# Optimization experiments

Hardware: AMD Instinct MI355X
Metric: run time of the kernel (lower is better)

## Reference

```python
import jax, jax.numpy as jnp
import numpy as np

N = 100000      # nodes
E = 1600000     # edges (avg degree 16)
N_IN, N_HID, N_OUT = 512, 256, 64
HOP = 10


def setup_inputs() -> dict:
    key = jax.random.key(0)
    k = jax.random.split(key, 8)
    x = jax.random.normal(k[0], (N, N_IN), dtype=jnp.float32)
    edge_row = jax.random.randint(k[1], (E,), 0, N, dtype=jnp.int64)
    edge_col = jax.random.randint(k[2], (E,), 0, N, dtype=jnp.int64)
    # values ~ 1/avg_degree, mimicking normalized adjacency
    edge_vals = jax.random.uniform(k[3], (E,), dtype=jnp.float32) * 0.0625
    W1 = jax.random.normal(k[4], (N_HID, N_IN), dtype=jnp.float32) * (1.0 / np.sqrt(N_IN))
    b1 = jnp.zeros((N_HID,), dtype=jnp.float32)
    W2 = jax.random.normal(k[5], (N_OUT, N_HID), dtype=jnp.float32) * (1.0 / np.sqrt(N_HID))
    b2 = jnp.zeros((N_OUT,), dtype=jnp.float32)
    s = jax.random.normal(k[6], (N_OUT, 1), dtype=jnp.float32) * 0.1
    return {"x": x, "edge_row": edge_row, "edge_col": edge_col,
            "edge_vals": edge_vals, "W1": W1, "b1": b1, "W2": W2,
            "b2": b2, "s": s}


def reference(x, edge_row, edge_col, edge_vals, W1, b1, W2, b2, s):
    # MLP transform (dropout=0 / eval mode)
    h = jax.nn.relu(x @ W1.T + b1)          # [N, N_HID]
    h = h @ W2.T + b2                        # [N, N_OUT]
    # multi-hop sparse propagation: h_{k+1} = A @ h_k  (COO SpMM)
    outs = [h]
    for _ in range(HOP):
        msg = edge_vals[:, None] * h[edge_col]                       # [E, N_OUT]
        h = jax.ops.segment_sum(msg, edge_row, num_segments=N)       # [N, N_OUT]
        outs.append(h)
    H = jnp.stack(outs, axis=1)              # [N, HOP+1, N_OUT]
    # sigmoid hop-attention: S = sigmoid(H @ s), out = S^T H
    S = jax.nn.sigmoid(jnp.einsum('nkf,fo->nk', H, s))  # [N, HOP+1]
    out = jnp.einsum('nk,nkf->nf', S, H)     # [N, N_OUT]
    return out
```

## Files before the change

kernel.cpp:

```cpp
#include <hip/hip_runtime.h>
#include <hip/hip_bf16.h>

#define NIN  512
#define NHID 256
#define NOUT 64
#define HOPS 10

typedef __attribute__((ext_vector_type(8))) short bf16x8;
typedef __attribute__((ext_vector_type(4))) float f32x4;

__device__ __forceinline__ unsigned short f2bf(float f) {
    unsigned u = __float_as_uint(f);
    u += 0x7FFFu + ((u >> 16) & 1u);
    return (unsigned short)(u >> 16);
}
__device__ __forceinline__ unsigned pk2(float a, float b) {
    return (unsigned)f2bf(a) | ((unsigned)f2bf(b) << 16);
}
__device__ __forceinline__ float bflo(unsigned g) { return __uint_as_float(g << 16); }
__device__ __forceinline__ float bfhi(unsigned g) { return __uint_as_float(g & 0xFFFF0000u); }

__global__ void k_preconv(const float* __restrict__ W1, const float* __restrict__ W2,
                          unsigned short* __restrict__ W1f, unsigned short* __restrict__ W2f)
{
    const int i = blockIdx.x * 256 + threadIdx.x;
    if (i < NHID * NIN) {
        const int j = i & 7, l = (i >> 3) & 63, fi = i >> 9;
        const int ks = fi >> 4, w = (fi >> 2) & 3, nf = fi & 3;
        const int col = w * 64 + nf * 16 + (l & 15);
        const int k   = ks * 32 + ((l >> 4) << 3) + j;
        W1f[i] = f2bf(W1[col * NIN + k]);
    }
    if (i < NOUT * NHID) {
        const int j = i & 7, l = (i >> 3) & 63, fi = i >> 9;
        const int ks = fi >> 2, nf = fi & 3;
        const int col = nf * 16 + (l & 15);
        const int k   = ks * 32 + ((j >> 2) << 4) + ((l >> 4) << 2) + (j & 3);
        W2f[i] = f2bf(W2[col * NHID + k]);
    }
}

__global__ __launch_bounds__(256, 2) void mlp_kernel(
    const float* __restrict__ x, const unsigned short* __restrict__ W1f,
    const float* __restrict__ b1, const unsigned short* __restrict__ W2f,
    const float* __restrict__ b2, const float* __restrict__ s,
    unsigned* __restrict__ hpack, float* __restrict__ sigbuf, int n)
{
    __shared__ __align__(16) char smem[50432];
    short* B2L  = (short*)smem;
    short* BX   = (short*)(smem + 32768);
    float* H0L  = (float*)(smem + 32768);
    float* SIGL = (float*)(smem + 50176);

    const int t  = threadIdx.x;
    const int w  = t >> 6, lz = t & 63;
    const int row0 = blockIdx.x * 64;

    const int srow = t >> 2;
    int xrow = row0 + srow; if (xrow >= n) xrow = n - 1;
    const float4* xp = (const float4*)(x + (size_t)xrow * NIN);
    const int q4a = t & 3, q4b = (t & 3) + 4;

    f32x4 acc[4][4];
    #pragma unroll
    for (int a = 0; a < 4; ++a)
        #pragma unroll
        for (int b = 0; b < 4; ++b) acc[a][b] = (f32x4)(0.f);

    auto xwrite = [&](int b, float4 va, float4 vb) {
        unsigned long long pa = (unsigned long long)pk2(va.x, va.y)
                              | ((unsigned long long)pk2(va.z, va.w) << 32);
        unsigned long long pb = (unsigned long long)pk2(vb.x, vb.y)
                              | ((unsigned long long)pk2(vb.z, vb.w) << 32);
        *(unsigned long long*)&BX[(((((b << 2) + (srow >> 4)) << 6)
            + ((srow & 15) | ((q4a >> 1) << 4))) << 3) + ((q4a & 1) << 2)] = pa;
        *(unsigned long long*)&BX[(((((b << 2) + (srow >> 4)) << 6)
            + ((srow & 15) | ((q4b >> 1) << 4))) << 3) + ((q4b & 1) << 2)] = pb;
    };
    auto compute = [&](int b, int kt) {
        bf16x8 xf[4], wf[4];
        #pragma unroll
        for (int nfn = 0; nfn < 4; ++nfn)
            xf[nfn] = *(const bf16x8*)&BX[((((b << 2) + nfn) << 6) + lz) << 3];
        const unsigned short* wp = W1f + ((size_t)kt << 13) + (w << 11) + (lz << 3);
        #pragma unroll
        for (int hf = 0; hf < 4; ++hf)
            wf[hf] = *(const bf16x8*)(wp + (hf << 9));
        #pragma unroll
        for (int nfn = 0; nfn < 4; ++nfn)
            #pragma unroll
            for (int hf = 0; hf < 4; ++hf)
                acc[nfn][hf] = __builtin_amdgcn_mfma_f32_16x16x32_bf16(
                    wf[hf], xf[nfn], acc[nfn][hf], 0, 0, 0);
    };

    {
        float4 xa = xp[q4a], xb = xp[q4b];
        xwrite(0, xa, xb);
    }
    __syncthreads();

    #pragma unroll 1
    for (int kt = 0; kt < 16; ++kt) {
        const int b = kt & 1;
        float4 nxa, nxb;
        if (kt < 15) {
            nxa = xp[((kt + 1) << 3) + q4a];
            nxb = xp[((kt + 1) << 3) + q4b];
        }
        compute(b, kt);
        if (kt < 15) xwrite(b ^ 1, nxa, nxb);
        __syncthreads();
    }

    {
        float4 b1q[4];
        #pragma unroll
        for (int hf = 0; hf < 4; ++hf)
            b1q[hf] = *(const float4*)(b1 + (w << 6) + (hf << 4) + ((lz >> 4) << 2));
        #pragma unroll
        for (int nfn = 0; nfn < 4; ++nfn) {
            #pragma unroll
            for (int cl = 0; cl < 2; ++cl) {
                f32x4 a0 = acc[nfn][2 * cl], a1 = acc[nfn][2 * cl + 1];
                float4 c0 = b1q[2 * cl], c1 = b1q[2 * cl + 1];
                uint4 pv;
                pv.x = pk2(fmaxf(a0.x + c0.x, 0.f), fmaxf(a0.y + c0.y, 0.f));
                pv.y = pk2(fmaxf(a0.z + c0.z, 0.f), fmaxf(a0.w + c0.w, 0.f));
                pv.z = pk2(fmaxf(a1.x + c1.x, 0.f), fmaxf(a1.y + c1.y, 0.f));
                pv.w = pk2(fmaxf(a1.z + c1.z, 0.f), fmaxf(a1.w + c1.w, 0.f));
                *(uint4*)&B2L[((((nfn << 3) + (w << 1) + cl) << 6) + lz) << 3] = pv;
            }
        }
    }
    __syncthreads();

    f32x4 acc2[4];
    #pragma unroll
    for (int nf2 = 0; nf2 < 4; ++nf2) acc2[nf2] = (f32x4)(0.f);

    #pragma unroll
    for (int c = 0; c < 8; ++c) {
        bf16x8 hfrag = *(const bf16x8*)&B2L[((((w << 3) + c) << 6) + lz) << 3];
        #pragma unroll
        for (int nf2 = 0; nf2 < 4; ++nf2) {
            bf16x8 wfrag = *(const bf16x8*)(W2f + (((c << 2) + nf2) << 9) + (lz << 3));
            acc2[nf2] = __builtin_amdgcn_mfma_f32_16x16x32_bf16(
                wfrag, hfrag, acc2[nf2], 0, 0, 0);
        }
    }

    {
        float dot = 0.f;
        #pragma unroll
        for (int nf2 = 0; nf2 < 4; ++nf2) {
            float4 bq = *(const float4*)(b2 + (nf2 << 4) + ((lz >> 4) << 2));
            float4 qv = *(const float4*)(s  + (nf2 << 4) + ((lz >> 4) << 2));
            acc2[nf2].x += bq.x; acc2[nf2].y += bq.y;
            acc2[nf2].z += bq.z; acc2[nf2].w += bq.w;
            dot += acc2[nf2].x * qv.x + acc2[nf2].y * qv.y
                 + acc2[nf2].z * qv.z + acc2[nf2].w * qv.w;
        }
        dot += __shfl_xor(dot, 16);
        dot += __shfl_xor(dot, 32);
        const float sig = 1.f / (1.f + expf(-dot));
        if (lz < 16) SIGL[(w << 4) + lz] = sig;
        const int mloc = (w << 4) + (lz & 15);
        #pragma unroll
        for (int nf2 = 0; nf2 < 4; ++nf2) {
            float4 hv; hv.x = acc2[nf2].x; hv.y = acc2[nf2].y;
            hv.z = acc2[nf2].z; hv.w = acc2[nf2].w;
            *(float4*)&H0L[mloc * 68 + (nf2 << 4) + ((lz >> 4) << 2)] = hv;
        }
    }
    __syncthreads();

    {
        const int m = t >> 2, q = t & 3;
        const int g = row0 + m;
        if (g < n) {
            unsigned* hp = hpack + (size_t)g * 32 + (q << 3);
            #pragma unroll
            for (int i = 0; i < 16; i += 4) {
                float4 hv = *(const float4*)&H0L[m * 68 + (q << 4) + i];
                uint2 pv;
                pv.x = pk2(hv.x, hv.y);
                pv.y = pk2(hv.z, hv.w);
                *(uint2*)(hp + (i >> 1)) = pv;
            }
        }
        if (t < 64 && row0 + t < n) sigbuf[row0 + t] = SIGL[t];
    }
}

__global__ void k_count(const int* __restrict__ erow, int* __restrict__ deg, int e) {
    int i = blockIdx.x * 256 + threadIdx.x;
    if (i < e) atomicAdd(&deg[erow[i]], 1);
}

__global__ void k_scan1(const int* __restrict__ deg, int* __restrict__ rp,
                        int* __restrict__ bsum, int nv) {
    __shared__ int sm[256];
    const int i = blockIdx.x * 256 + threadIdx.x;
    const int v = (i < nv) ? deg[i] : 0;
    sm[threadIdx.x] = v;
    __syncthreads();
    for (int off = 1; off < 256; off <<= 1) {
        int tv = (threadIdx.x >= off) ? sm[threadIdx.x - off] : 0;
        __syncthreads();
        sm[threadIdx.x] += tv;
        __syncthreads();
    }
    if (i < nv) rp[i] = sm[threadIdx.x] - v;
    if (threadIdx.x == 255) bsum[blockIdx.x] = sm[255];
}

__global__ void k_scan2(int* __restrict__ bsum, int nb) {
    __shared__ int sm[512];
    const int tid = threadIdx.x;
    const int v = (tid < nb) ? bsum[tid] : 0;
    sm[tid] = v;
    __syncthreads();
    for (int off = 1; off < 512; off <<= 1) {
        int tv = (tid >= off) ? sm[tid - off] : 0;
        __syncthreads();
        sm[tid] += tv;
        __syncthreads();
    }
    if (tid < nb) bsum[tid] = sm[tid] - v;
}

__global__ void k_scan3(int* __restrict__ rp, int* __restrict__ cur,
                        const int* __restrict__ bsum, int nv, int e) {
    const int i = blockIdx.x * 256 + threadIdx.x;
    if (i < nv) {
        const int vv = rp[i] + bsum[blockIdx.x];
        rp[i]  = vv;
        cur[i] = vv;
    }
    if (i == 0) rp[nv] = e;
}

__global__ void k_scatter(const int* __restrict__ erow, const int* __restrict__ ecol,
                          const float* __restrict__ ev, int* __restrict__ cur,
                          unsigned long long* __restrict__ cpack, int e) {
    const int i = blockIdx.x * 256 + threadIdx.x;
    if (i < e) {
        const int r = erow[i];
        const int p = atomicAdd(&cur[r], 1);
        cpack[p] = ((unsigned long long)__float_as_uint(ev[i]) << 32)
                 | (unsigned)ecol[i];
    }
}

__global__ __launch_bounds__(256) void hop_kernel(
    const unsigned* __restrict__ h_in, unsigned* __restrict__ h_out,
    const int* __restrict__ row_ptr, const unsigned long long* __restrict__ cpack,
    const float* __restrict__ s, float* __restrict__ sig_out, int n)
{
    const int t  = threadIdx.x;
    const int sl = t & 31;
    const int node = (blockIdx.x * 256 + t) >> 5;
    if (node >= n) return;
    const int start = row_ptr[node];
    const int end   = row_ptr[node + 1];
    float a0 = 0.f, a1 = 0.f;
    for (int base = start; base < end; base += 32) {
        const int idx = base + sl;
        unsigned long long pc = (idx < end) ? cpack[idx] : 0ULL;
        int   c = (int)(unsigned)pc;
        float v = __uint_as_float((unsigned)(pc >> 32));
        const int cnt = min(32, end - base);
        int e = 0;
        for (; e + 4 <= cnt; e += 4) {
            int   c0 = __shfl(c, e, 32),     c1 = __shfl(c, e + 1, 32);
            int   c2 = __shfl(c, e + 2, 32), c3 = __shfl(c, e + 3, 32);
            float v0 = __shfl(v, e, 32),     v1 = __shfl(v, e + 1, 32);
            float v2 = __shfl(v, e + 2, 32), v3 = __shfl(v, e + 3, 32);
            unsigned g0 = h_in[(size_t)c0 * 32 + sl];
            unsigned g1 = h_in[(size_t)c1 * 32 + sl];
            unsigned g2 = h_in[(size_t)c2 * 32 + sl];
            unsigned g3 = h_in[(size_t)c3 * 32 + sl];
            a0 = fmaf(v0, bflo(g0), a0); a1 = fmaf(v0, bfhi(g0), a1);
            a0 = fmaf(v1, bflo(g1), a0); a1 = fmaf(v1, bfhi(g1), a1);
            a0 = fmaf(v2, bflo(g2), a0); a1 = fmaf(v2, bfhi(g2), a1);
            a0 = fmaf(v3, bflo(g3), a0); a1 = fmaf(v3, bfhi(g3), a1);
        }
        for (; e < cnt; ++e) {
            int   cc = __shfl(c, e, 32);
            float vv = __shfl(v, e, 32);
            unsigned g = h_in[(size_t)cc * 32 + sl];
            a0 = fmaf(vv, bflo(g), a0); a1 = fmaf(vv, bfhi(g), a1);
        }
    }
    const float2 sv = ((const float2*)s)[sl];
    float tv = a0 * sv.x + a1 * sv.y;
    #pragma unroll
    for (int off = 16; off > 0; off >>= 1) tv += __shfl_xor(tv, off, 32);
    h_out[(size_t)node * 32 + sl] = pk2(a0, a1);
    if (sl == 0) sig_out[node] = 1.f / (1.f + expf(-tv));
}

__global__ __launch_bounds__(256) void k_combine(
    const unsigned* __restrict__ hbuf, const float* __restrict__ sigbuf,
    float* __restrict__ out, int n)
{
    const int gid  = blockIdx.x * 256 + threadIdx.x;
    const int node = gid >> 5, sl = gid & 31;
    if (node >= n) return;
    float o0 = 0.f, o1 = 0.f;
    #pragma unroll
    for (int k = 0; k <= HOPS; ++k) {
        const unsigned g = hbuf[(size_t)k * n * 32 + (size_t)node * 32 + sl];
        const float sg = sigbuf[(size_t)k * n + node];
        o0 = fmaf(sg, bflo(g), o0);
        o1 = fmaf(sg, bfhi(g), o1);
    }
    float2 ov; ov.x = o0; ov.y = o1;
    ((float2*)out)[(size_t)node * 32 + sl] = ov;
}

extern "C" void kernel_launch(void* const* d_in, const int* in_sizes, int n_in,
                              void* d_out, int out_size, void* d_ws, size_t ws_size,
                              hipStream_t stream)
{
    const float* x  = (const float*)d_in[0];
    const int*   er = (const int*)  d_in[1];
    const int*   ec = (const int*)  d_in[2];
    const float* ev = (const float*)d_in[3];
    const float* W1 = (const float*)d_in[4];
    const float* b1 = (const float*)d_in[5];
    const float* W2 = (const float*)d_in[6];
    const float* b2 = (const float*)d_in[7];
    const float* s  = (const float*)d_in[8];
    float* out = (float*)d_out;

    const int n = in_sizes[0] / NIN;
    const int e = in_sizes[1];

    char* w = (char*)d_ws;
    auto carve = [&](size_t bytes) { char* p = w; w += (bytes + 255) & ~(size_t)255; return p; };
    unsigned* hbuf   = (unsigned*)carve((size_t)(HOPS + 1) * n * 32 * 4);
    float*    sigbuf = (float*)   carve((size_t)(HOPS + 1) * n * 4);
    int*      deg    = (int*)     carve((size_t)n * 4);
    int*      rp     = (int*)     carve(((size_t)n + 1) * 4);
    int*      cur    = (int*)     carve((size_t)n * 4);
    unsigned long long* cpack = (unsigned long long*)carve((size_t)e * 8);
    int*      bsum   = (int*)     carve(1024 * 4);
    unsigned short* W1f = (unsigned short*)carve((size_t)NHID * NIN * 2);
    unsigned short* W2f = (unsigned short*)carve((size_t)NOUT * NHID * 2);

    hipMemsetAsync(deg, 0, (size_t)n * 4, stream);

    k_preconv<<<(NHID * NIN + 255) / 256, 256, 0, stream>>>(W1, W2, W1f, W2f);

    const int mgrid = (n + 63) / 64;
    mlp_kernel<<<mgrid, 256, 0, stream>>>(x, W1f, b1, W2f, b2, s,
                                          hbuf, sigbuf, n);

    const int eg = (e + 255) / 256;
    const int nb = (n + 255) / 256;
    k_count  <<<eg, 256, 0, stream>>>(er, deg, e);
    k_scan1  <<<nb, 256, 0, stream>>>(deg, rp, bsum, n);
    k_scan2  <<<1, 512, 0, stream>>>(bsum, nb);
    k_scan3  <<<nb, 256, 0, stream>>>(rp, cur, bsum, n, e);
    k_scatter<<<eg, 256, 0, stream>>>(er, ec, ev, cur, cpack, e);

    const int hgrid = ((size_t)n * 32 + 255) / 256;
    for (int hop = 0; hop < HOPS; ++hop) {
        hop_kernel<<<hgrid, 256, 0, stream>>>(
            hbuf + (size_t)hop * n * 32, hbuf + (size_t)(hop + 1) * n * 32,
            rp, cpack, s, sigbuf + (size_t)(hop + 1) * n, n);
    }

    k_combine<<<hgrid, 256, 0, stream>>>(hbuf, sigbuf, out, n);
}
```

Before: 626.0 us.

## Bucket edges by row range before CSR scatter to localize atomics and writes

Builds the CSR with a two-pass scatter. Edges are first appended into 64 coarse row buckets (2048 rows each) using block-local histograms and per-bucket global cursors. The fine atomic scatter into cpack then walks this bucketed stream, so its atomics and writes touch a small row window at a time instead of random addresses. The cost is an extra 16-byte-per-edge intermediate buffer and one more pass over the edges. The change also raises the MLP kernel's launch-bounds occupancy hint from 2 to 3, which may increase register pressure.

```diff
diff --git a/kernel.cpp b/kernel.cpp
--- a/kernel.cpp
+++ b/kernel.cpp
@@ -5,6 +5,7 @@
 #define NHID 256
 #define NOUT 64
 #define HOPS 10
+#define NB   64
 
 typedef __attribute__((ext_vector_type(8))) short bf16x8;
 typedef __attribute__((ext_vector_type(4))) float f32x4;
@@ -40,7 +41,7 @@
     }
 }
 
-__global__ __launch_bounds__(256, 2) void mlp_kernel(
+__global__ __launch_bounds__(256, 3) void mlp_kernel(
     const float* __restrict__ x, const unsigned short* __restrict__ W1f,
     const float* __restrict__ b1, const unsigned short* __restrict__ W2f,
     const float* __restrict__ b2, const float* __restrict__ s,
@@ -193,9 +194,20 @@
     }
 }
 
-__global__ void k_count(const int* __restrict__ erow, int* __restrict__ deg, int e) {
-    int i = blockIdx.x * 256 + threadIdx.x;
-    if (i < e) atomicAdd(&deg[erow[i]], 1);
+__global__ void k_count_hist(const int* __restrict__ erow, int* __restrict__ deg,
+                             int* __restrict__ bcnt, int e) {
+    __shared__ int lh[NB];
+    const int t = threadIdx.x;
+    if (t < NB) lh[t] = 0;
+    __syncthreads();
+    const int i = blockIdx.x * 256 + t;
+    if (i < e) {
+        const int r = erow[i];
+        atomicAdd(&deg[r], 1);
+        atomicAdd(&lh[r >> 11], 1);
+    }
+    __syncthreads();
+    if (t < NB && lh[t]) atomicAdd(&bcnt[t], lh[t]);
 }
 
 __global__ void k_scan1(const int* __restrict__ deg, int* __restrict__ rp,
@@ -215,7 +227,8 @@
     if (threadIdx.x == 255) bsum[blockIdx.x] = sm[255];
 }
 
-__global__ void k_scan2(int* __restrict__ bsum, int nb) {
+__global__ void k_scan2(int* __restrict__ bsum, int nb,
+                        const int* __restrict__ bcnt, int* __restrict__ bcur) {
     __shared__ int sm[512];
     const int tid = threadIdx.x;
     const int v = (tid < nb) ? bsum[tid] : 0;
@@ -228,6 +241,16 @@
         __syncthreads();
     }
     if (tid < nb) bsum[tid] = sm[tid] - v;
+    if (tid < NB) {
+        int bv = bcnt[tid];
+        int x = bv;
+        #pragma unroll
+        for (int off = 1; off < 64; off <<= 1) {
+            int y = __shfl_up(x, off);
+            if (tid >= off) x += y;
+        }
+        bcur[tid] = x - bv;
+    }
 }
 
 __global__ void k_scan3(int* __restrict__ rp, int* __restrict__ cur,
@@ -241,15 +264,44 @@
     if (i == 0) rp[nv] = e;
 }
 
-__global__ void k_scatter(const int* __restrict__ erow, const int* __restrict__ ecol,
-                          const float* __restrict__ ev, int* __restrict__ cur,
-                          unsigned long long* __restrict__ cpack, int e) {
+__global__ void k_bappend(const int* __restrict__ erow, const int* __restrict__ ecol,
+                          const float* __restrict__ ev, int* __restrict__ bcur,
+                          uint4* __restrict__ brec, int e) {
+    __shared__ int lh[NB];
+    __shared__ int lbase[NB];
+    __shared__ int lrank[NB];
+    const int t = threadIdx.x;
+    if (t < NB) lh[t] = 0;
+    __syncthreads();
+    const int i = blockIdx.x * 256 + t;
+    const bool valid = i < e;
+    int r = 0, b = 0;
+    if (valid) { r = erow[i]; b = r >> 11; atomicAdd(&lh[b], 1); }
+    __syncthreads();
+    if (t < NB) {
+        const int c = lh[t];
+        lbase[t] = c ? atomicAdd(&bcur[t], c) : 0;
+        lrank[t] = 0;
+    }
+    __syncthreads();
+    if (valid) {
+        const int rk = atomicAdd(&lrank[b], 1);
+        uint4 rec;
+        rec.x = (unsigned)r;
+        rec.y = (unsigned)ecol[i];
+        rec.z = __float_as_uint(ev[i]);
+        rec.w = 0;
+        brec[lbase[b] + rk] = rec;
+    }
+}
+
+__global__ void k_scatter2(const uint4* __restrict__ brec, int* __restrict__ cur,
+                           unsigned long long* __restrict__ cpack, int e) {
     const int i = blockIdx.x * 256 + threadIdx.x;
     if (i < e) {
-        const int r = erow[i];
-        const int p = atomicAdd(&cur[r], 1);
-        cpack[p] = ((unsigned long long)__float_as_uint(ev[i]) << 32)
-                 | (unsigned)ecol[i];
+        const uint4 rec = brec[i];
+        const int p = atomicAdd(&cur[rec.x], 1);
+        cpack[p] = ((unsigned long long)rec.z << 32) | rec.y;
     }
 }
 
@@ -346,11 +398,15 @@
     int*      rp     = (int*)     carve(((size_t)n + 1) * 4);
     int*      cur    = (int*)     carve((size_t)n * 4);
     unsigned long long* cpack = (unsigned long long*)carve((size_t)e * 8);
+    uint4*    brec   = (uint4*)   carve((size_t)e * 16);
     int*      bsum   = (int*)     carve(1024 * 4);
+    int*      bcnt   = (int*)     carve(NB * 4);
+    int*      bcur   = (int*)     carve(NB * 4);
     unsigned short* W1f = (unsigned short*)carve((size_t)NHID * NIN * 2);
     unsigned short* W2f = (unsigned short*)carve((size_t)NOUT * NHID * 2);
 
     hipMemsetAsync(deg, 0, (size_t)n * 4, stream);
+    hipMemsetAsync(bcnt, 0, NB * 4, stream);
 
     k_preconv<<<(NHID * NIN + 255) / 256, 256, 0, stream>>>(W1, W2, W1f, W2f);
 
@@ -360,11 +416,12 @@
 
     const int eg = (e + 255) / 256;
     const int nb = (n + 255) / 256;
-    k_count  <<<eg, 256, 0, stream>>>(er, deg, e);
-    k_scan1  <<<nb, 256, 0, stream>>>(deg, rp, bsum, n);
-    k_scan2  <<<1, 512, 0, stream>>>(bsum, nb);
-    k_scan3  <<<nb, 256, 0, stream>>>(rp, cur, bsum, n, e);
-    k_scatter<<<eg, 256, 0, stream>>>(er, ec, ev, cur, cpack, e);
+    k_count_hist<<<eg, 256, 0, stream>>>(er, deg, bcnt, e);
+    k_scan1     <<<nb, 256, 0, stream>>>(deg, rp, bsum, n);
+    k_scan2     <<<1, 512, 0, stream>>>(bsum, nb, bcnt, bcur);
+    k_scan3     <<<nb, 256, 0, stream>>>(rp, cur, bsum, n, e);
+    k_bappend   <<<eg, 256, 0, stream>>>(er, ec, ev, bcur, brec, e);
+    k_scatter2  <<<eg, 256, 0, stream>>>(brec, cur, cpack, e);
 
     const int hgrid = ((size_t)n * 32 + 255) / 256;
     for (int hop = 0; hop < HOPS; ++hop) {
```

New measurement: 846.7 us. +35.3%, slower.

## Move hop-attention sigmoid into combine kernel and prefetch W1 fragments

Applied to the files above, without the earlier changes.

The per-hop sigmoid score computation is removed from the MLP and hop kernels and recomputed in the final combine kernel from the stored bf16 hidden states. This drops the sigbuf buffer and its writes and reads, and takes the reductions out of the hop loop. The combine kernel now does eleven warp reductions and exps per node, and the sigmoid inputs are bf16-rounded values rather than fp32 accumulators. The MLP kernel also software-prefetches the next W1 fragments into registers and raises launch bounds from 2 to 3 blocks, which may increase register pressure.

```diff
diff --git a/kernel.cpp b/kernel.cpp
--- a/kernel.cpp
+++ b/kernel.cpp
@@ -40,17 +40,16 @@
     }
 }
 
-__global__ __launch_bounds__(256, 2) void mlp_kernel(
+__global__ __launch_bounds__(256, 3) void mlp_kernel(
     const float* __restrict__ x, const unsigned short* __restrict__ W1f,
     const float* __restrict__ b1, const unsigned short* __restrict__ W2f,
-    const float* __restrict__ b2, const float* __restrict__ s,
-    unsigned* __restrict__ hpack, float* __restrict__ sigbuf, int n)
-{
-    __shared__ __align__(16) char smem[50432];
+    const float* __restrict__ b2,
+    unsigned* __restrict__ hpack, int n)
+{
+    __shared__ __align__(16) char smem[50176];
     short* B2L  = (short*)smem;
     short* BX   = (short*)(smem + 32768);
     float* H0L  = (float*)(smem + 32768);
-    float* SIGL = (float*)(smem + 50176);
 
     const int t  = threadIdx.x;
     const int w  = t >> 6, lz = t & 63;
@@ -77,15 +76,17 @@
         *(unsigned long long*)&BX[(((((b << 2) + (srow >> 4)) << 6)
             + ((srow & 15) | ((q4b >> 1) << 4))) << 3) + ((q4b & 1) << 2)] = pb;
     };
-    auto compute = [&](int b, int kt) {
-        bf16x8 xf[4], wf[4];
+    auto wload = [&](int kt, bf16x8* wf) {
+        const unsigned short* wp = W1f + ((size_t)kt << 13) + (w << 11) + (lz << 3);
+        #pragma unroll
+        for (int hf = 0; hf < 4; ++hf)
+            wf[hf] = *(const bf16x8*)(wp + (hf << 9));
+    };
+    auto compute = [&](int b, const bf16x8* wf) {
+        bf16x8 xf[4];
         #pragma unroll
         for (int nfn = 0; nfn < 4; ++nfn)
             xf[nfn] = *(const bf16x8*)&BX[((((b << 2) + nfn) << 6) + lz) << 3];
-        const unsigned short* wp = W1f + ((size_t)kt << 13) + (w << 11) + (lz << 3);
-        #pragma unroll
-        for (int hf = 0; hf < 4; ++hf)
-            wf[hf] = *(const bf16x8*)(wp + (hf << 9));
         #pragma unroll
         for (int nfn = 0; nfn < 4; ++nfn)
             #pragma unroll
@@ -94,8 +95,10 @@
                     wf[hf], xf[nfn], acc[nfn][hf], 0, 0, 0);
     };
 
+    bf16x8 wfc[4], wfn[4];
     {
         float4 xa = xp[q4a], xb = xp[q4b];
+        wload(0, wfc);
         xwrite(0, xa, xb);
     }
     __syncthreads();
@@ -107,9 +110,14 @@
         if (kt < 15) {
             nxa = xp[((kt + 1) << 3) + q4a];
             nxb = xp[((kt + 1) << 3) + q4b];
-        }
-        compute(b, kt);
-        if (kt < 15) xwrite(b ^ 1, nxa, nxb);
+            wload(kt + 1, wfn);
+        }
+        compute(b, wfc);
+        if (kt < 15) {
+            xwrite(b ^ 1, nxa, nxb);
+            #pragma unroll
+            for (int hf = 0; hf < 4; ++hf) wfc[hf] = wfn[hf];
+        }
         __syncthreads();
     }
 
@@ -151,25 +159,13 @@
     }
 
     {
-        float dot = 0.f;
+        const int mloc = (w << 4) + (lz & 15);
         #pragma unroll
         for (int nf2 = 0; nf2 < 4; ++nf2) {
             float4 bq = *(const float4*)(b2 + (nf2 << 4) + ((lz >> 4) << 2));
-            float4 qv = *(const float4*)(s  + (nf2 << 4) + ((lz >> 4) << 2));
-            acc2[nf2].x += bq.x; acc2[nf2].y += bq.y;
-            acc2[nf2].z += bq.z; acc2[nf2].w += bq.w;
-            dot += acc2[nf2].x * qv.x + acc2[nf2].y * qv.y
-                 + acc2[nf2].z * qv.z + acc2[nf2].w * qv.w;
-        }
-        dot += __shfl_xor(dot, 16);
-        dot += __shfl_xor(dot, 32);
-        const float sig = 1.f / (1.f + expf(-dot));
-        if (lz < 16) SIGL[(w << 4) + lz] = sig;
-        const int mloc = (w << 4) + (lz & 15);
-        #pragma unroll
-        for (int nf2 = 0; nf2 < 4; ++nf2) {
-            float4 hv; hv.x = acc2[nf2].x; hv.y = acc2[nf2].y;
-            hv.z = acc2[nf2].z; hv.w = acc2[nf2].w;
+            float4 hv;
+            hv.x = acc2[nf2].x + bq.x; hv.y = acc2[nf2].y + bq.y;
+            hv.z = acc2[nf2].z + bq.z; hv.w = acc2[nf2].w + bq.w;
             *(float4*)&H0L[mloc * 68 + (nf2 << 4) + ((lz >> 4) << 2)] = hv;
         }
     }
@@ -189,7 +185,6 @@
                 *(uint2*)(hp + (i >> 1)) = pv;
             }
         }
-        if (t < 64 && row0 + t < n) sigbuf[row0 + t] = SIGL[t];
     }
 }
 
@@ -256,7 +251,7 @@
 __global__ __launch_bounds__(256) void hop_kernel(
     const unsigned* __restrict__ h_in, unsigned* __restrict__ h_out,
     const int* __restrict__ row_ptr, const unsigned long long* __restrict__ cpack,
-    const float* __restrict__ s, float* __restrict__ sig_out, int n)
+    int n)
 {
     const int t  = threadIdx.x;
     const int sl = t & 31;
@@ -293,28 +288,28 @@
             a0 = fmaf(vv, bflo(g), a0); a1 = fmaf(vv, bfhi(g), a1);
         }
     }
-    const float2 sv = ((const float2*)s)[sl];
-    float tv = a0 * sv.x + a1 * sv.y;
-    #pragma unroll
-    for (int off = 16; off > 0; off >>= 1) tv += __shfl_xor(tv, off, 32);
     h_out[(size_t)node * 32 + sl] = pk2(a0, a1);
-    if (sl == 0) sig_out[node] = 1.f / (1.f + expf(-tv));
 }
 
 __global__ __launch_bounds__(256) void k_combine(
-    const unsigned* __restrict__ hbuf, const float* __restrict__ sigbuf,
+    const unsigned* __restrict__ hbuf, const float* __restrict__ s,
     float* __restrict__ out, int n)
 {
     const int gid  = blockIdx.x * 256 + threadIdx.x;
     const int node = gid >> 5, sl = gid & 31;
     if (node >= n) return;
+    const float2 sv = ((const float2*)s)[sl];
     float o0 = 0.f, o1 = 0.f;
     #pragma unroll
     for (int k = 0; k <= HOPS; ++k) {
         const unsigned g = hbuf[(size_t)k * n * 32 + (size_t)node * 32 + sl];
-        const float sg = sigbuf[(size_t)k * n + node];
-        o0 = fmaf(sg, bflo(g), o0);
-        o1 = fmaf(sg, bfhi(g), o1);
+        const float lo = bflo(g), hi = bfhi(g);
+        float tv = lo * sv.x + hi * sv.y;
+        #pragma unroll
+        for (int off = 16; off > 0; off >>= 1) tv += __shfl_xor(tv, off, 32);
+        const float sg = 1.f / (1.f + expf(-tv));
+        o0 = fmaf(sg, lo, o0);
+        o1 = fmaf(sg, hi, o1);
     }
     float2 ov; ov.x = o0; ov.y = o1;
     ((float2*)out)[(size_t)node * 32 + sl] = ov;
@@ -341,7 +336,6 @@
     char* w = (char*)d_ws;
     auto carve = [&](size_t bytes) { char* p = w; w += (bytes + 255) & ~(size_t)255; return p; };
     unsigned* hbuf   = (unsigned*)carve((size_t)(HOPS + 1) * n * 32 * 4);
-    float*    sigbuf = (float*)   carve((size_t)(HOPS + 1) * n * 4);
     int*      deg    = (int*)     carve((size_t)n * 4);
     int*      rp     = (int*)     carve(((size_t)n + 1) * 4);
     int*      cur    = (int*)     carve((size_t)n * 4);
@@ -355,8 +349,7 @@
     k_preconv<<<(NHID * NIN + 255) / 256, 256, 0, stream>>>(W1, W2, W1f, W2f);
 
     const int mgrid = (n + 63) / 64;
-    mlp_kernel<<<mgrid, 256, 0, stream>>>(x, W1f, b1, W2f, b2, s,
-                                          hbuf, sigbuf, n);
+    mlp_kernel<<<mgrid, 256, 0, stream>>>(x, W1f, b1, W2f, b2, hbuf, n);
 
     const int eg = (e + 255) / 256;
     const int nb = (n + 255) / 256;
@@ -370,8 +363,8 @@
     for (int hop = 0; hop < HOPS; ++hop) {
         hop_kernel<<<hgrid, 256, 0, stream>>>(
             hbuf + (size_t)hop * n * 32, hbuf + (size_t)(hop + 1) * n * 32,
-            rp, cpack, s, sigbuf + (size_t)(hop + 1) * n, n);
-    }
-
-    k_combine<<<hgrid, 256, 0, stream>>>(hbuf, sigbuf, out, n);
-}
+            rp, cpack, n);
+    }
+
+    k_combine<<<hgrid, 256, 0, stream>>>(hbuf, s, out, n);
+}
```

Result: no change. 631.0 us (+0.8%).
